# Performance work log

Measured on AMD Instinct MI355X. Metric: run time of the kernel, lower is better.

Reference implementation:

```python
import jax, jax.numpy as jnp
import numpy as np

B, C_IN, N = 4, 128, 4096
E = 131072           # nnz edges in the sparse adjacency
C_OUT = 128          # module out_channels
C_CONV = C_OUT - 1   # add_counts=True steals one channel for degree counts


def setup_inputs() -> dict:
    key = jax.random.key(0)
    kx, ki, kj, kw, kb = jax.random.split(key, 5)
    x = jax.random.normal(kx, (B, C_IN, N), dtype=jnp.float32)
    # edge list (i, j) for each nonzero of the sparse adjacency
    idx_i = jax.random.randint(ki, (E,), 0, N)
    idx_j = jax.random.randint(kj, (E,), 0, N)
    # Conv1d(in=C_IN, out=C_CONV, kernel_size=2, stride=2) weights
    W = jax.random.normal(kw, (C_CONV, C_IN, 2), dtype=jnp.float32) * 0.05
    b = jax.random.normal(kb, (C_CONV,), dtype=jnp.float32) * 0.05
    return {"x": x, "W": W, "b": b, "idx_i": idx_i, "idx_j": idx_j}


def reference(x, W, b, idx_i, idx_j):
    # _conv: x @ adj_pw.T is a gather of the two endpoints of every edge
    # (adj_pw row 2k selects node idx_i[k], row 2k+1 selects node idx_j[k]).
    # Conv1d(kernel=2, stride=2) then mixes the interleaved endpoint pair:
    #   pair[b,o,e] = sum_c W[o,c,0]*x[b,c,i_e] + W[o,c,1]*x[b,c,j_e] + b[o]
    xi = x[:, :, idx_i]                                   # [B, C, E]
    xj = x[:, :, idx_j]                                   # [B, C, E]
    pair = (jnp.einsum('oc,bce->boe', W[:, :, 0], xi)
            + jnp.einsum('oc,bce->boe', W[:, :, 1], xj)
            + b[None, :, None])                           # [B, C_CONV, E]
    # x @ adj_pw[::2, :] scatter-adds each edge's output to its first endpoint
    n = x.shape[2]
    y = jnp.zeros((x.shape[0], pair.shape[1], n), dtype=x.dtype)
    y = y.at[:, :, idx_i].add(pair)                       # [B, C_CONV, N]
    # adj_sum = adj.to_dense().sum(dim=0): in-degree over columns j
    deg = jnp.zeros((n,), dtype=x.dtype).at[idx_j].add(1.0)
    # normalize: divide by degree clamped to >= 1
    y = y / jnp.where(deg == 0, 1.0, deg)
    # add_counts: append raw degree as an extra channel
    counts = jnp.broadcast_to(deg[None, None, :], (y.shape[0], 1, n))
    return jnp.concatenate([y, counts], axis=1)           # [B, C_OUT, N]
```

## Files before the change

### kernel.cpp

```cpp
#include <hip/hip_runtime.h>
#include <cstdint>
#include <cstddef>

#define BATCH   4
#define CIN     128
#define NN      4096
#define EE      131072
#define CCONV   127
#define NBC     512
#define MAXDEG  128
#define CPAD    16

typedef __attribute__((ext_vector_type(8))) short short8;
typedef __attribute__((ext_vector_type(8))) unsigned short ushort8;
typedef __attribute__((ext_vector_type(4))) float f32x4;

__device__ __forceinline__ unsigned short f2bf(float f) {
    unsigned int u = __float_as_uint(f);
    return (unsigned short)((u + 0x7FFFu + ((u >> 16) & 1u)) >> 16);
}
__device__ __forceinline__ float bf2f(unsigned short h) {
    return __uint_as_float((unsigned int)h << 16);
}

__global__ __launch_bounds__(256) void k_pre(const float* __restrict__ x,
                                             unsigned short* __restrict__ xT,
                                             const float* __restrict__ W,
                                             unsigned short* __restrict__ WTb,
                                             const int* __restrict__ idx_i,
                                             const int* __restrict__ idx_j,
                                             int* __restrict__ cursor,
                                             unsigned short* __restrict__ elist,
                                             int* __restrict__ deg) {
    const int bid = blockIdx.x;
    const int tid = threadIdx.x;
    if (bid < 256) {
        __shared__ float tile[128][65];
        const int b  = bid & 3;
        const int n0 = (bid >> 2) * 64;
        const int rl = tid >> 4;
        const int l4 = (tid & 15) * 4;
        const float* xb = x + (size_t)b * CIN * NN + n0 + l4;
#pragma unroll
        for (int it = 0; it < 8; ++it) {
            const int c = it * 16 + rl;
            const float4 v = *(const float4*)(xb + (size_t)c * NN);
            tile[c][l4 + 0] = v.x;
            tile[c][l4 + 1] = v.y;
            tile[c][l4 + 2] = v.z;
            tile[c][l4 + 3] = v.w;
        }
        __syncthreads();
        const int l = tid & 63;
#pragma unroll
        for (int it = 0; it < 16; ++it) {
            const int n = it * 4 + (tid >> 6);
            ushort2 r;
            r.x = f2bf(tile[2 * l + 0][n]);
            r.y = f2bf(tile[2 * l + 1][n]);
            *(ushort2*)(xT + (size_t)(n0 + n) * NBC + b * CIN + 2 * l) = r;
        }
    } else if (bid < 768) {
        const int e  = (bid - 256) * 256 + tid;
        const int ni = idx_i[e];
        const int nj = idx_j[e];
        const int pos = atomicAdd(&cursor[ni * CPAD], 1);
        elist[(size_t)ni * MAXDEG + pos] = (unsigned short)nj;
        atomicAdd(&deg[nj * CPAD], 1);
    } else {
        const int t = (bid - 768) * 256 + tid;
        const int o = t >> 8;
        const int k = t & 255;
        float v = 0.0f;
        if (o < CCONV) v = W[((size_t)o * CIN + (k & 127)) * 2 + (k >> 7)];
        WTb[t] = f2bf(v);
    }
}

__global__ __launch_bounds__(256) void k_final(const unsigned short* __restrict__ xT,
                                               const unsigned short* __restrict__ WTb,
                                               const float* __restrict__ bias,
                                               const unsigned short* __restrict__ elist,
                                               const int* __restrict__ cnt_i,
                                               const int* __restrict__ deg,
                                               float* __restrict__ out) {
    __shared__ short Af[512 * 8];
    __shared__ float cntf[16], invd[16], degf[16], biasf[128];
    __shared__ int   cnti[16];

    const int tid = threadIdx.x;
    const int b   = blockIdx.y;
    const int n0  = blockIdx.x * 16;

    if (tid < 16) {
        const int c = cnt_i[(n0 + tid) * CPAD];
        const int d = deg[(n0 + tid) * CPAD];
        cnti[tid] = c;
        cntf[tid] = (float)c;
        degf[tid] = (float)d;
        invd[tid] = (d == 0) ? 1.0f : 1.0f / (float)d;
    } else if (tid >= 64 && tid < 192) {
        const int o = tid - 64;
        biasf[o] = (o < CCONV) ? bias[o] : 0.0f;
    }
    __syncthreads();

    const int lane = tid & 63;
    const int w    = tid >> 6;

    {
        const int ns = lane >> 4;
        const int j  = w * 4 + ns;
        const int c0 = (lane & 15) * 8;
        const unsigned short* xb = xT + b * CIN + c0;
        const int dn = cnti[j];
        const unsigned short* erow = elist + (size_t)(n0 + j) * MAXDEG;
        float acc[8] = {0, 0, 0, 0, 0, 0, 0, 0};
        int k = 0;
        for (; k + 8 <= dn; k += 8) {
            const ushort8 i8 = *(const ushort8*)(erow + k);
            ushort8 u[8];
#pragma unroll
            for (int t = 0; t < 8; ++t)
                u[t] = *(const ushort8*)(xb + (size_t)i8[t] * NBC);
#pragma unroll
            for (int t = 0; t < 8; ++t)
#pragma unroll
                for (int q = 0; q < 8; ++q) acc[q] += bf2f(u[t][q]);
        }
        for (; k < dn; ++k) {
            const ushort8 u = *(const ushort8*)(xb + (size_t)erow[k] * NBC);
#pragma unroll
            for (int q = 0; q < 8; ++q) acc[q] += bf2f(u[q]);
        }
        short8 p;
#pragma unroll
        for (int q = 0; q < 8; ++q) p[q] = (short)f2bf(acc[q]);
        const int kt   = 4 + (c0 >> 5);
        const int g    = (c0 >> 3) & 3;
        const int unit = kt * 64 + 16 * g + j;
        *(short8*)&Af[unit * 8] = p;
    }

    {
        const int L  = tid & 63;
        const int kt = tid >> 6;
        const int j  = L & 15;
        const int k0 = kt * 32 + (L >> 4) * 8;
        const short8 a = *(const short8*)(xT + (size_t)(n0 + j) * NBC + b * CIN + k0);
        const float sc = cntf[j];
        short8 p;
#pragma unroll
        for (int q = 0; q < 8; ++q)
            p[q] = (short)f2bf(bf2f((unsigned short)a[q]) * sc);
        *(short8*)&Af[(kt * 64 + L) * 8] = p;
    }
    __syncthreads();

    const int m = lane & 15;
    const int g = lane >> 4;

    f32x4 acc0 = (f32x4){0.0f, 0.0f, 0.0f, 0.0f};
    f32x4 acc1 = (f32x4){0.0f, 0.0f, 0.0f, 0.0f};

    const unsigned short* B0 = WTb + (size_t)(w * 32 + m) * 256;
    const unsigned short* B1 = B0 + 16 * 256;

#pragma unroll
    for (int kt = 0; kt < 8; ++kt) {
        const int k0 = kt * 32 + g * 8;
        const short8 b0 = *(const short8*)(B0 + k0);
        const short8 b1 = *(const short8*)(B1 + k0);
        const short8 a  = *(const short8*)&Af[(kt * 64 + lane) * 8];
        acc0 = __builtin_amdgcn_mfma_f32_16x16x32_bf16(a, b0, acc0, 0, 0, 0);
        acc1 = __builtin_amdgcn_mfma_f32_16x16x32_bf16(a, b1, acc1, 0, 0, 0);
    }

#pragma unroll
    for (int nt = 0; nt < 2; ++nt) {
        const f32x4 a = nt ? acc1 : acc0;
        const int o = w * 32 + nt * 16 + m;
        if (o >= CCONV) continue;
        const float bo = biasf[o];
        float* orow = out + ((size_t)b * 128 + o) * NN + n0;
        const int j0 = g * 4;
        float4 r;
        r.x = (a[0] + cntf[j0 + 0] * bo) * invd[j0 + 0];
        r.y = (a[1] + cntf[j0 + 1] * bo) * invd[j0 + 1];
        r.z = (a[2] + cntf[j0 + 2] * bo) * invd[j0 + 2];
        r.w = (a[3] + cntf[j0 + 3] * bo) * invd[j0 + 3];
        *(float4*)(orow + j0) = r;
    }
    if (tid < 16)
        out[((size_t)b * 128 + CCONV) * NN + n0 + tid] = degf[tid];
}

extern "C" void kernel_launch(void* const* d_in, const int* in_sizes, int n_in,
                              void* d_out, int out_size, void* d_ws, size_t ws_size,
                              hipStream_t stream) {
    const float* x    = (const float*)d_in[0];
    const float* W    = (const float*)d_in[1];
    const float* bias = (const float*)d_in[2];
    const int* idx_i  = (const int*)d_in[3];
    const int* idx_j  = (const int*)d_in[4];
    float* out = (float*)d_out;

    char* ws = (char*)d_ws;
    unsigned short* xT     = (unsigned short*)(ws);
    unsigned short* elist  = (unsigned short*)(ws + 4194304);
    unsigned short* WTb    = (unsigned short*)(ws + 5242880);
    int*            cursor = (int*)(ws + 5308416);
    int*            deg    = (int*)(ws + 5570560);

    hipMemsetAsync(cursor, 0, 524288, stream);

    k_pre<<<896, 256, 0, stream>>>(x, xT, W, WTb, idx_i, idx_j, cursor, elist, deg);
    k_final<<<dim3(NN / 16, BATCH), 256, 0, stream>>>(xT, WTb, bias, elist, cursor, deg, out);
}
```

Measured before the change: 102.0 us.

## Fuse pre-pass and final kernels into one persistent kernel with grid barrier

```diff
diff --git a/kernel.cpp b/kernel.cpp
--- a/kernel.cpp
+++ b/kernel.cpp
@@ -10,6 +10,7 @@
 #define NBC     512
 #define MAXDEG  128
 #define CPAD    16
+#define GRID    1024
 
 typedef __attribute__((ext_vector_type(8))) short short8;
 typedef __attribute__((ext_vector_type(8))) unsigned short ushort8;
@@ -23,19 +24,30 @@
     return __uint_as_float((unsigned int)h << 16);
 }
 
-__global__ __launch_bounds__(256) void k_pre(const float* __restrict__ x,
-                                             unsigned short* __restrict__ xT,
-                                             const float* __restrict__ W,
-                                             unsigned short* __restrict__ WTb,
-                                             const int* __restrict__ idx_i,
-                                             const int* __restrict__ idx_j,
-                                             int* __restrict__ cursor,
-                                             unsigned short* __restrict__ elist,
-                                             int* __restrict__ deg) {
+__global__ __launch_bounds__(256, 4) void k_all(const float* __restrict__ x,
+                                                unsigned short* __restrict__ xT,
+                                                const float* __restrict__ W,
+                                                unsigned short* __restrict__ WTb,
+                                                const int* __restrict__ idx_i,
+                                                const int* __restrict__ idx_j,
+                                                int* __restrict__ cd,
+                                                unsigned short* __restrict__ elist,
+                                                int* __restrict__ bar,
+                                                const float* __restrict__ bias,
+                                                float* __restrict__ out) {
+    __shared__ union {
+        float tile[128][65];
+        struct {
+            short Af[512 * 8];
+            float cntf[16], invd[16], degf[16], biasf[128];
+            int   cnti[16];
+        } p2;
+    } sm;
+
     const int bid = blockIdx.x;
     const int tid = threadIdx.x;
+
     if (bid < 256) {
-        __shared__ float tile[128][65];
         const int b  = bid & 3;
         const int n0 = (bid >> 2) * 64;
         const int rl = tid >> 4;
@@ -45,10 +57,10 @@
         for (int it = 0; it < 8; ++it) {
             const int c = it * 16 + rl;
             const float4 v = *(const float4*)(xb + (size_t)c * NN);
-            tile[c][l4 + 0] = v.x;
-            tile[c][l4 + 1] = v.y;
-            tile[c][l4 + 2] = v.z;
-            tile[c][l4 + 3] = v.w;
+            sm.tile[c][l4 + 0] = v.x;
+            sm.tile[c][l4 + 1] = v.y;
+            sm.tile[c][l4 + 2] = v.z;
+            sm.tile[c][l4 + 3] = v.w;
         }
         __syncthreads();
         const int l = tid & 63;
@@ -56,18 +68,18 @@
         for (int it = 0; it < 16; ++it) {
             const int n = it * 4 + (tid >> 6);
             ushort2 r;
-            r.x = f2bf(tile[2 * l + 0][n]);
-            r.y = f2bf(tile[2 * l + 1][n]);
+            r.x = f2bf(sm.tile[2 * l + 0][n]);
+            r.y = f2bf(sm.tile[2 * l + 1][n]);
             *(ushort2*)(xT + (size_t)(n0 + n) * NBC + b * CIN + 2 * l) = r;
         }
     } else if (bid < 768) {
         const int e  = (bid - 256) * 256 + tid;
         const int ni = idx_i[e];
         const int nj = idx_j[e];
-        const int pos = atomicAdd(&cursor[ni * CPAD], 1);
+        const int pos = atomicAdd(&cd[ni * CPAD], 1);
         elist[(size_t)ni * MAXDEG + pos] = (unsigned short)nj;
-        atomicAdd(&deg[nj * CPAD], 1);
-    } else {
+        atomicAdd(&cd[nj * CPAD + 1], 1);
+    } else if (bid < 896) {
         const int t = (bid - 768) * 256 + tid;
         const int o = t >> 8;
         const int k = t & 255;
@@ -75,33 +87,31 @@
         if (o < CCONV) v = W[((size_t)o * CIN + (k & 127)) * 2 + (k >> 7)];
         WTb[t] = f2bf(v);
     }
-}
-
-__global__ __launch_bounds__(256) void k_final(const unsigned short* __restrict__ xT,
-                                               const unsigned short* __restrict__ WTb,
-                                               const float* __restrict__ bias,
-                                               const unsigned short* __restrict__ elist,
-                                               const int* __restrict__ cnt_i,
-                                               const int* __restrict__ deg,
-                                               float* __restrict__ out) {
-    __shared__ short Af[512 * 8];
-    __shared__ float cntf[16], invd[16], degf[16], biasf[128];
-    __shared__ int   cnti[16];
-
-    const int tid = threadIdx.x;
-    const int b   = blockIdx.y;
-    const int n0  = blockIdx.x * 16;
+
+    __threadfence();
+    __syncthreads();
+    if (tid == 0) {
+        __hip_atomic_fetch_add(bar, 1, __ATOMIC_ACQ_REL, __HIP_MEMORY_SCOPE_AGENT);
+        while (__hip_atomic_load(bar, __ATOMIC_ACQUIRE, __HIP_MEMORY_SCOPE_AGENT) < GRID) {
+            __builtin_amdgcn_s_sleep(2);
+        }
+    }
+    __syncthreads();
+    __threadfence();
+
+    const int b  = bid & 3;
+    const int n0 = (bid >> 2) * 16;
 
     if (tid < 16) {
-        const int c = cnt_i[(n0 + tid) * CPAD];
-        const int d = deg[(n0 + tid) * CPAD];
-        cnti[tid] = c;
-        cntf[tid] = (float)c;
-        degf[tid] = (float)d;
-        invd[tid] = (d == 0) ? 1.0f : 1.0f / (float)d;
+        const int c = cd[(n0 + tid) * CPAD];
+        const int d = cd[(n0 + tid) * CPAD + 1];
+        sm.p2.cnti[tid] = c;
+        sm.p2.cntf[tid] = (float)c;
+        sm.p2.degf[tid] = (float)d;
+        sm.p2.invd[tid] = (d == 0) ? 1.0f : 1.0f / (float)d;
     } else if (tid >= 64 && tid < 192) {
         const int o = tid - 64;
-        biasf[o] = (o < CCONV) ? bias[o] : 0.0f;
+        sm.p2.biasf[o] = (o < CCONV) ? bias[o] : 0.0f;
     }
     __syncthreads();
 
@@ -113,7 +123,7 @@
         const int j  = w * 4 + ns;
         const int c0 = (lane & 15) * 8;
         const unsigned short* xb = xT + b * CIN + c0;
-        const int dn = cnti[j];
+        const int dn = sm.p2.cnti[j];
         const unsigned short* erow = elist + (size_t)(n0 + j) * MAXDEG;
         float acc[8] = {0, 0, 0, 0, 0, 0, 0, 0};
         int k = 0;
@@ -139,7 +149,7 @@
         const int kt   = 4 + (c0 >> 5);
         const int g    = (c0 >> 3) & 3;
         const int unit = kt * 64 + 16 * g + j;
-        *(short8*)&Af[unit * 8] = p;
+        *(short8*)&sm.p2.Af[unit * 8] = p;
     }
 
     {
@@ -148,12 +158,12 @@
         const int j  = L & 15;
         const int k0 = kt * 32 + (L >> 4) * 8;
         const short8 a = *(const short8*)(xT + (size_t)(n0 + j) * NBC + b * CIN + k0);
-        const float sc = cntf[j];
+        const float sc = sm.p2.cntf[j];
         short8 p;
 #pragma unroll
         for (int q = 0; q < 8; ++q)
             p[q] = (short)f2bf(bf2f((unsigned short)a[q]) * sc);
-        *(short8*)&Af[(kt * 64 + L) * 8] = p;
+        *(short8*)&sm.p2.Af[(kt * 64 + L) * 8] = p;
     }
     __syncthreads();
 
@@ -171,7 +181,7 @@
         const int k0 = kt * 32 + g * 8;
         const short8 b0 = *(const short8*)(B0 + k0);
         const short8 b1 = *(const short8*)(B1 + k0);
-        const short8 a  = *(const short8*)&Af[(kt * 64 + lane) * 8];
+        const short8 a  = *(const short8*)&sm.p2.Af[(kt * 64 + lane) * 8];
         acc0 = __builtin_amdgcn_mfma_f32_16x16x32_bf16(a, b0, acc0, 0, 0, 0);
         acc1 = __builtin_amdgcn_mfma_f32_16x16x32_bf16(a, b1, acc1, 0, 0, 0);
     }
@@ -181,18 +191,18 @@
         const f32x4 a = nt ? acc1 : acc0;
         const int o = w * 32 + nt * 16 + m;
         if (o >= CCONV) continue;
-        const float bo = biasf[o];
+        const float bo = sm.p2.biasf[o];
         float* orow = out + ((size_t)b * 128 + o) * NN + n0;
         const int j0 = g * 4;
         float4 r;
-        r.x = (a[0] + cntf[j0 + 0] * bo) * invd[j0 + 0];
-        r.y = (a[1] + cntf[j0 + 1] * bo) * invd[j0 + 1];
-        r.z = (a[2] + cntf[j0 + 2] * bo) * invd[j0 + 2];
-        r.w = (a[3] + cntf[j0 + 3] * bo) * invd[j0 + 3];
+        r.x = (a[0] + sm.p2.cntf[j0 + 0] * bo) * sm.p2.invd[j0 + 0];
+        r.y = (a[1] + sm.p2.cntf[j0 + 1] * bo) * sm.p2.invd[j0 + 1];
+        r.z = (a[2] + sm.p2.cntf[j0 + 2] * bo) * sm.p2.invd[j0 + 2];
+        r.w = (a[3] + sm.p2.cntf[j0 + 3] * bo) * sm.p2.invd[j0 + 3];
         *(float4*)(orow + j0) = r;
     }
     if (tid < 16)
-        out[((size_t)b * 128 + CCONV) * NN + n0 + tid] = degf[tid];
+        out[((size_t)b * 128 + CCONV) * NN + n0 + tid] = sm.p2.degf[tid];
 }
 
 extern "C" void kernel_launch(void* const* d_in, const int* in_sizes, int n_in,
@@ -206,14 +216,14 @@
     float* out = (float*)d_out;
 
     char* ws = (char*)d_ws;
-    unsigned short* xT     = (unsigned short*)(ws);
-    unsigned short* elist  = (unsigned short*)(ws + 4194304);
-    unsigned short* WTb    = (unsigned short*)(ws + 5242880);
-    int*            cursor = (int*)(ws + 5308416);
-    int*            deg    = (int*)(ws + 5570560);
-
-    hipMemsetAsync(cursor, 0, 524288, stream);
-
-    k_pre<<<896, 256, 0, stream>>>(x, xT, W, WTb, idx_i, idx_j, cursor, elist, deg);
-    k_final<<<dim3(NN / 16, BATCH), 256, 0, stream>>>(xT, WTb, bias, elist, cursor, deg, out);
-}
+    unsigned short* xT    = (unsigned short*)(ws);
+    unsigned short* elist = (unsigned short*)(ws + 4194304);
+    unsigned short* WTb   = (unsigned short*)(ws + 5242880);
+    int*            cd    = (int*)(ws + 5308416);
+    int*            bar   = (int*)(ws + 5570560);
+
+    hipMemsetAsync(cd, 0, 262208, stream);
+
+    k_all<<<GRID, 256, 0, stream>>>(x, xT, W, WTb, idx_i, idx_j, cd, elist,
+                                    bar, bias, out);
+}
```

New measurement: 307.9 us. +202.0%, slower.
